# Optimization experiments

Hardware: AMD Instinct MI355X
Metric: run time of the kernel (lower is better)

The kernel has to match this reference:

```python
import math
import numpy as np
import jax, jax.numpy as jnp

L_MAX = 3
N_NODES = 16384
C_IN = 128
C_OUT = 128
IRREPS_DIM = (L_MAX + 1) ** 2  # 16 (dims 1+3+5+7, offset of l is l*l)


def _su2_cg(j1, j2, j3):
    """Complex-basis SU(2) Clebsch-Gordan <j1 m1 j2 m2 | j3 m3> (Racah formula)."""
    f = math.factorial
    C = np.zeros((2 * j1 + 1, 2 * j2 + 1, 2 * j3 + 1))
    for m1 in range(-j1, j1 + 1):
        for m2 in range(-j2, j2 + 1):
            m3 = m1 + m2
            if abs(m3) > j3:
                continue
            pref = math.sqrt((2 * j3 + 1) * f(j3 + j1 - j2) * f(j3 - j1 + j2) * f(j1 + j2 - j3) / f(j1 + j2 + j3 + 1))
            pref *= math.sqrt(f(j3 + m3) * f(j3 - m3) * f(j1 - m1) * f(j1 + m1) * f(j2 - m2) * f(j2 + m2))
            s = 0.0
            for k in range(0, j1 + j2 + 1):
                d = [k, j1 + j2 - j3 - k, j1 - m1 - k, j2 + m2 - k, j3 - j2 + m1 + k, j3 - j1 - m2 + k]
                if any(x < 0 for x in d):
                    continue
                s += (-1.0) ** k / (f(d[0]) * f(d[1]) * f(d[2]) * f(d[3]) * f(d[4]) * f(d[5]))
            C[m1 + j1, m2 + j2, m3 + j3] = pref * s
    return C


def _q(l):
    """Real->complex spherical-harmonic change of basis (e3nn convention, incl. (-i)^l)."""
    q = np.zeros((2 * l + 1, 2 * l + 1), dtype=complex)
    r2 = 1.0 / math.sqrt(2.0)
    for m in range(-l, 0):
        q[l + m, l + abs(m)] = r2
        q[l + m, l - abs(m)] = -1j * r2
    q[l, l] = 1.0
    for m in range(1, l + 1):
        q[l + m, l + abs(m)] = (-1) ** m * r2
        q[l + m, l - abs(m)] = 1j * (-1) ** m * r2
    return (-1j) ** l * q


def _real_cg(l1, l2, l3):
    """Real-basis Clebsch-Gordan tensor, shape (2l1+1, 2l2+1, 2l3+1). Real-valued."""
    C = _su2_cg(l1, l2, l3).astype(complex)
    W = np.einsum('ai,bj,ck,abc->ijk', _q(l1), _q(l2), _q(l3), C)
    return np.real(W).astype(np.float32)


# All triangle-allowed coupling paths (l1, l2, l_out); 34 paths for L_MAX=3.
PATHS = [(l1, l2, lo)
         for lo in range(L_MAX + 1)
         for l1 in range(L_MAX + 1)
         for l2 in range(L_MAX + 1)
         if abs(l1 - l2) <= lo <= l1 + l2]
NUM_PATHS = len(PATHS)
_counts = {}
for (_l1, _l2, _lo) in PATHS:
    _counts[_lo] = _counts.get(_lo, 0) + 1
# path_norm: divide each path by sqrt(#paths feeding its output irrep)
PATH_SCALE = [1.0 / math.sqrt(_counts[lo]) for (_, _, lo) in PATHS]
CG = {(l1, l2, lo): _real_cg(l1, l2, lo) for (l1, l2, lo) in PATHS}


def setup_inputs() -> dict:
    key = jax.random.key(0)
    k1, k2, k3 = jax.random.split(key, 3)
    input1 = jax.random.normal(k1, (N_NODES, IRREPS_DIM, C_IN), dtype=jnp.float32)
    input2 = jax.random.normal(k2, (N_NODES, IRREPS_DIM), dtype=jnp.float32)
    # uv-mode weight: (num_paths, channels_in, channels_out); fan-in init std=1/sqrt(C_IN)
    weight = jax.random.normal(k3, (NUM_PATHS, C_IN, C_OUT), dtype=jnp.float32) * (C_IN ** -0.5)
    return {"input1": input1, "input2": input2, "weight": weight}


def _forward(x1, x2, w):
    N = x1.shape[0]
    out = jnp.zeros((N, IRREPS_DIM, w.shape[-1]), dtype=x1.dtype)
    for p, (l1, l2, lo) in enumerate(PATHS):
        Cp = jnp.asarray(CG[(l1, l2, lo)], dtype=x1.dtype)      # (2l1+1, 2l2+1, 2lo+1)
        a = x1[:, l1 * l1:(l1 + 1) ** 2, :]                      # (N, 2l1+1, U)
        b = x2[:, l2 * l2:(l2 + 1) ** 2]                         # (N, 2l2+1)
        t = jnp.einsum('nau,nb,abc->ncu', a, b, Cp)              # (N, 2lo+1, U)
        o = jnp.einsum('ncu,uv->ncv', t, w[p]) * PATH_SCALE[p]   # (N, 2lo+1, V)
        out = out.at[:, lo * lo:(lo + 1) ** 2, :].add(o)
    return out


def reference(input1, input2, weight):
    return _forward(input1, input2, weight)
```

## Files before the change

kernel.cpp:

```cpp
#include <hip/hip_runtime.h>
#include <cstddef>

namespace so3 {

constexpr int IRR  = 16;
constexpr int CIN  = 128;
constexpr int COUT = 128;
constexpr int NP   = 34;
constexpr int NNODES = 16384;
constexpr int MT   = 16;

constexpr int H_L1[NP] = {0,1,2,3, 0,1,1,1,2,2,2,3,3, 0,1,1,1,2,2,2,2,3,3,3, 0,1,1,2,2,2,3,3,3,3};
constexpr int H_L2[NP] = {0,1,2,3, 1,0,1,2,1,2,3,2,3, 2,1,2,3,0,1,2,3,1,2,3, 3,2,3,1,2,3,0,1,2,3};
constexpr int H_START[4] = {0,4,13,24};
constexpr int H_CNT[4]   = {4,9,11,10};

constexpr double cfac(int n){ double r=1.0; for(int i=2;i<=n;++i) r *= (double)i; return r; }
constexpr double csqrt_(double x){
  if(x <= 0.0) return 0.0;
  double r = x < 1.0 ? 1.0 : x;
  for(int i=0;i<60;++i) r = 0.5*(r + x/r);
  return r;
}
constexpr double m1pow(int k){ return (k & 1) ? -1.0 : 1.0; }

struct CD { double re, im; };
constexpr CD cmul(CD a, CD b){ return CD{a.re*b.re - a.im*b.im, a.re*b.im + a.im*b.re}; }

struct CGDense { double v[7][7][7]; };
constexpr CGDense su2_cg(int j1,int j2,int j3){
  CGDense C{};
  for(int m1=-j1;m1<=j1;++m1){
    for(int m2=-j2;m2<=j2;++m2){
      int m3 = m1+m2;
      if(m3 < -j3 || m3 > j3) continue;
      double pref = csqrt_((2*j3+1) * cfac(j3+j1-j2)*cfac(j3-j1+j2)*cfac(j1+j2-j3)/cfac(j1+j2+j3+1));
      pref *= csqrt_(cfac(j3+m3)*cfac(j3-m3)*cfac(j1-m1)*cfac(j1+m1)*cfac(j2-m2)*cfac(j2+m2));
      double s = 0.0;
      for(int k=0;k<=j1+j2;++k){
        int d0=k, d1=j1+j2-j3-k, d2=j1-m1-k, d3=j2+m2-k, d4=j3-j2+m1+k, d5=j3-j1-m2+k;
        if(d0<0||d1<0||d2<0||d3<0||d4<0||d5<0) continue;
        s += m1pow(k)/(cfac(d0)*cfac(d1)*cfac(d2)*cfac(d3)*cfac(d4)*cfac(d5));
      }
      C.v[m1+j1][m2+j2][m3+j3] = pref*s;
    }
  }
  return C;
}

struct QMat { CD v[7][7]; };
constexpr QMat qmat(int l){
  QMat q{};
  const double r2 = 1.0/csqrt_(2.0);
  for(int m=-l;m<0;++m){
    q.v[l+m][l-m] = CD{r2, 0.0};
    q.v[l+m][l+m] = CD{0.0, -r2};
  }
  q.v[l][l] = CD{1.0, 0.0};
  for(int m=1;m<=l;++m){
    double sgn = m1pow(m);
    q.v[l+m][l+m] = CD{sgn*r2, 0.0};
    q.v[l+m][l-m] = CD{0.0, sgn*r2};
  }
  CD ph = CD{1.0, 0.0};
  int lm = l & 3;
  if(lm==1) ph = CD{0.0,-1.0};
  else if(lm==2) ph = CD{-1.0,0.0};
  else if(lm==3) ph = CD{0.0, 1.0};
  for(int i=0;i<2*l+1;++i)
    for(int j=0;j<2*l+1;++j)
      q.v[i][j] = cmul(q.v[i][j], ph);
  return q;
}

struct RealCG { double v[7][7][7]; };
constexpr RealCG real_cg(int l1,int l2,int l3){
  RealCG W{};
  const CGDense C = su2_cg(l1,l2,l3);
  const QMat q1 = qmat(l1), q2 = qmat(l2), q3 = qmat(l3);
  for(int i=0;i<2*l1+1;++i){
    int alist[2] = {i, 2*l1-i};
    int na = (alist[1]==alist[0]) ? 1 : 2;
    for(int j=0;j<2*l2+1;++j){
      int blist[2] = {j, 2*l2-j};
      int nb = (blist[1]==blist[0]) ? 1 : 2;
      for(int k=0;k<2*l3+1;++k){
        int clist[2] = {k, 2*l3-k};
        int nc = (clist[1]==clist[0]) ? 1 : 2;
        double re = 0.0;
        for(int ai=0;ai<na;++ai) for(int bi=0;bi<nb;++bi) for(int ci=0;ci<nc;++ci){
          int a=alist[ai], b=blist[bi], c=clist[ci];
          double cc = C.v[a][b][c];
          if(cc == 0.0) continue;
          CD t = cmul(cmul(q1.v[a][i], q2.v[b][j]), q3.v[c][k]);
          re += t.re * cc;
        }
        W.v[i][j][k] = re;
      }
    }
  }
  return W;
}

#define DECL_CG(n,a,b,c) constexpr RealCG CGP##n = real_cg(a,b,c);
DECL_CG(0,0,0,0)  DECL_CG(1,1,1,0)  DECL_CG(2,2,2,0)  DECL_CG(3,3,3,0)
DECL_CG(4,0,1,1)  DECL_CG(5,1,0,1)  DECL_CG(6,1,1,1)  DECL_CG(7,1,2,1)
DECL_CG(8,2,1,1)  DECL_CG(9,2,2,1)  DECL_CG(10,2,3,1) DECL_CG(11,3,2,1)
DECL_CG(12,3,3,1) DECL_CG(13,0,2,2) DECL_CG(14,1,1,2) DECL_CG(15,1,2,2)
DECL_CG(16,1,3,2) DECL_CG(17,2,0,2) DECL_CG(18,2,1,2) DECL_CG(19,2,2,2)
DECL_CG(20,2,3,2) DECL_CG(21,3,1,2) DECL_CG(22,3,2,2) DECL_CG(23,3,3,2)
DECL_CG(24,0,3,3) DECL_CG(25,1,2,3) DECL_CG(26,1,3,3) DECL_CG(27,2,1,3)
DECL_CG(28,2,2,3) DECL_CG(29,2,3,3) DECL_CG(30,3,0,3) DECL_CG(31,3,1,3)
DECL_CG(32,3,2,3) DECL_CG(33,3,3,3)
#undef DECL_CG

struct CGTable { float v[NP][7][7][7]; };
constexpr CGTable pack_cg(){
  const RealCG arr[NP] = {CGP0,CGP1,CGP2,CGP3,CGP4,CGP5,CGP6,CGP7,CGP8,CGP9,
                          CGP10,CGP11,CGP12,CGP13,CGP14,CGP15,CGP16,CGP17,CGP18,CGP19,
                          CGP20,CGP21,CGP22,CGP23,CGP24,CGP25,CGP26,CGP27,CGP28,CGP29,
                          CGP30,CGP31,CGP32,CGP33};
  CGTable t{};
  for(int p=0;p<NP;++p)
    for(int i=0;i<7;++i) for(int j=0;j<7;++j) for(int k=0;k<7;++k)
      t.v[p][i][j][k] = (float)arr[p].v[i][j][k];
  return t;
}

constexpr float PATH_SC[4] = {
  (float)(1.0/csqrt_((double)H_CNT[0])), (float)(1.0/csqrt_((double)H_CNT[1])),
  (float)(1.0/csqrt_((double)H_CNT[2])), (float)(1.0/csqrt_((double)H_CNT[3]))
};

}

__constant__ so3::CGTable c_cg = so3::pack_cg();

typedef __attribute__((ext_vector_type(8))) short bhalf8;
typedef __attribute__((ext_vector_type(4))) float floatx4;

__device__ __forceinline__ unsigned f2bf(float f){
  unsigned u = __builtin_bit_cast(unsigned, f);
  return (u + 0x7fffu + ((u>>16)&1u)) >> 16;
}

template<int LO, int PP>
__device__ __forceinline__ void path_iter(const int tid, const long n0,
    const float* __restrict__ x1, unsigned short* __restrict__ Tsh,
    float* __restrict__ gsh, const float* __restrict__ x2s,
    const unsigned short* __restrict__ wT,
    floatx4 (&acc)[16], bhalf8 (&bfrag)[4])
{
  using namespace so3;
  constexpr int NR  = 2*LO + 1;
  constexpr int CNT = H_CNT[LO];
  if constexpr (PP > CNT) { return; }
  else {
    const int lane = tid & 63;
    const int wv   = tid >> 6;
    const int lr   = lane & 15;
    const int lg   = lane >> 4;

    if constexpr (PP > 0) {
      constexpr int p = H_START[LO] + PP - 1;
      const unsigned short* wp = wT + p*16384 + (wv*16 + lr)*128 + lg*8;
      #pragma unroll
      for (int ks = 0; ks < 4; ++ks)
        bfrag[ks] = *(const bhalf8*)(wp + ks*32);
    }

    constexpr int n1_cur = (PP < CNT) ? (2*H_L1[H_START[LO] + (PP<CNT?PP:0)] + 1) : 1;
    float4 xf[n1_cur];
    const int bn = tid >> 5, u4 = tid & 31;
    if constexpr (PP < CNT) {
      constexpr int p  = H_START[LO] + PP;
      constexpr int l1 = H_L1[p];
      const float* x1p = x1 + ((size_t)(n0 + bn)*IRR + l1*l1)*CIN + u4*4;
      #pragma unroll
      for (int a = 0; a < n1_cur; ++a)
        xf[a] = *(const float4*)(x1p + a*CIN);
    }

    if constexpr (PP + 1 < CNT) {
      constexpr int p  = H_START[LO] + PP + 1;
      constexpr int l2 = H_L2[p];
      constexpr int n2 = 2*l2 + 1;
      constexpr int GT = NR*16*8;
      float* gout = gsh + ((PP+1)&1)*(7*16*8);
      #pragma unroll
      for (int e0 = 0; e0 < GT; e0 += 512) {
        const int e = e0 + tid;
        if (e < GT) {
          const int a = e & 7, n = (e >> 3) & 15, c = e >> 7;
          if (a < 2*H_L1[p] + 1) {
            float s = 0.f;
            #pragma unroll
            for (int b = 0; b < n2; ++b)
              s += c_cg.v[p][a][b][c] * x2s[n*16 + l2*l2 + b];
            gout[e] = s * PATH_SC[LO];
          }
        }
      }
    }

    if constexpr (PP < CNT) {
      const float* gin = gsh + (PP&1)*(7*16*8);
      char* Tbase = (char*)Tsh + (PP&1)*(7*16*128*2);
      #pragma unroll
      for (int c = 0; c < NR; ++c) {
        const float* g8 = gin + (c*16 + bn)*8;
        float garr[8];
        const float4 ga = *(const float4*)(g8);
        garr[0]=ga.x; garr[1]=ga.y; garr[2]=ga.z; garr[3]=ga.w;
        if constexpr (n1_cur > 4) {
          const float4 gb = *(const float4*)(g8 + 4);
          garr[4]=gb.x; garr[5]=gb.y; garr[6]=gb.z; garr[7]=gb.w;
        }
        float t0=0.f, t1=0.f, t2=0.f, t3=0.f;
        #pragma unroll
        for (int a = 0; a < n1_cur; ++a) {
          t0 += garr[a]*xf[a].x; t1 += garr[a]*xf[a].y;
          t2 += garr[a]*xf[a].z; t3 += garr[a]*xf[a].w;
        }
        uint2 o;
        o.x = f2bf(t0) | (f2bf(t1) << 16);
        o.y = f2bf(t2) | (f2bf(t3) << 16);
        const unsigned byte = ((unsigned)(((c*16 + bn)*128 + u4*4)*2)) ^ ((unsigned)((bn & 7) << 4));
        *(uint2*)(Tbase + byte) = o;
      }
    }

    if constexpr (PP > 0) {
      const char* Tbase = (const char*)Tsh + ((PP-1)&1)*(7*16*128*2);
      const unsigned xr = (unsigned)((lr & 7) << 4);
      #pragma unroll
      for (int c = 0; c < NR; ++c) {
        #pragma unroll
        for (int ks = 0; ks < 4; ++ks) {
          const unsigned byte = ((unsigned)((c*16 + lr)*256) + (unsigned)(ks*64 + lg*16)) ^ xr;
          bhalf8 av = *(const bhalf8*)(Tbase + byte);
          acc[LO*LO + c] = __builtin_amdgcn_mfma_f32_16x16x32_bf16(
              av, bfrag[ks], acc[LO*LO + c], 0, 0, 0);
        }
      }
    }
    __syncthreads();

    path_iter<LO, PP+1>(tid, n0, x1, Tsh, gsh, x2s, wT, acc, bfrag);
  }
}

template<int LO>
__device__ __forceinline__ void stage_a0(const int tid, float* __restrict__ gsh,
                                         const float* __restrict__ x2s)
{
  using namespace so3;
  constexpr int NR = 2*LO + 1;
  constexpr int p  = H_START[LO];
  constexpr int l1 = H_L1[p], l2 = H_L2[p];
  constexpr int n2 = 2*l2 + 1;
  constexpr int GT = NR*16*8;
  #pragma unroll
  for (int e0 = 0; e0 < GT; e0 += 512) {
    const int e = e0 + tid;
    if (e < GT) {
      const int a = e & 7, n = (e >> 3) & 15, c = e >> 7;
      if (a < 2*l1 + 1) {
        float s = 0.f;
        #pragma unroll
        for (int b = 0; b < n2; ++b)
          s += c_cg.v[p][a][b][c] * x2s[n*16 + l2*l2 + b];
        gsh[e] = s * PATH_SC[LO];
      }
    }
  }
}

__global__ __launch_bounds__(512, 4)
void so3_main(const float* __restrict__ x1, const float* __restrict__ x2,
              const unsigned short* __restrict__ wT, float* __restrict__ out)
{
  using namespace so3;
  __shared__ unsigned short Tsh[2*7*16*128];
  __shared__ float          gsh[2*7*16*8];
  __shared__ float          x2s[256];

  const int tid = threadIdx.x;
  const long n0 = (long)blockIdx.x * MT;

  if (tid < 256) x2s[tid] = x2[n0*16 + tid];
  __syncthreads();

  floatx4 acc[16];
  #pragma unroll
  for (int i = 0; i < 16; ++i) acc[i] = (floatx4){0.f,0.f,0.f,0.f};

  bhalf8 bfrag[4];

  stage_a0<0>(tid, gsh, x2s); __syncthreads();
  path_iter<0,0>(tid, n0, x1, Tsh, gsh, x2s, wT, acc, bfrag);
  stage_a0<1>(tid, gsh, x2s); __syncthreads();
  path_iter<1,0>(tid, n0, x1, Tsh, gsh, x2s, wT, acc, bfrag);
  stage_a0<2>(tid, gsh, x2s); __syncthreads();
  path_iter<2,0>(tid, n0, x1, Tsh, gsh, x2s, wT, acc, bfrag);
  stage_a0<3>(tid, gsh, x2s); __syncthreads();
  path_iter<3,0>(tid, n0, x1, Tsh, gsh, x2s, wT, acc, bfrag);

  const int lane = tid & 63, wv = tid >> 6, lr = lane & 15, lg = lane >> 4;
  const int v = wv*16 + lr;
  #pragma unroll
  for (int i = 0; i < 16; ++i) {
    #pragma unroll
    for (int r = 0; r < 4; ++r) {
      const long n = n0 + lg*4 + r;
      out[(n*16 + i)*128 + v] = acc[i][r];
    }
  }
}

__global__ void prep_wT(const float* __restrict__ w, unsigned short* __restrict__ wT)
{
  const int idx = blockIdx.x*256 + threadIdx.x;
  if (idx >= 34*128*128) return;
  const int p = idx >> 14, rem = idx & 16383, u = rem >> 7, v = rem & 127;
  wT[(p << 14) + (v << 7) + u] = (unsigned short)f2bf(w[idx]);
}

extern "C" void kernel_launch(void* const* d_in, const int* in_sizes, int n_in,
                              void* d_out, int out_size, void* d_ws, size_t ws_size,
                              hipStream_t stream)
{
  (void)in_sizes; (void)n_in; (void)out_size; (void)ws_size;
  const float* x1 = (const float*)d_in[0];
  const float* x2 = (const float*)d_in[1];
  const float* w  = (const float*)d_in[2];
  float* out = (float*)d_out;

  unsigned short* wT = (unsigned short*)d_ws;
  prep_wT<<<dim3(2176), dim3(256), 0, stream>>>(w, wT);
  so3_main<<<dim3(so3::NNODES / so3::MT), dim3(512), 0, stream>>>(x1, x2, wT, out);
}
```

Baseline: 317.4 us.

## Split kernel into two output-irrep pair launches with prefetched x1 and staged stores

The single fused kernel is split into two launches, one handling output irreps l=0 and l=3 and one handling l=1 and l=2, so each needs only 8 accumulator tiles instead of 16. This cuts register pressure and balances work between the two launches. x1 loads for the next path are now double-buffered in registers and issued ahead of the current path's compute. Output is staged through shared memory and written with coalesced float4 stores, and the block barrier is a custom waitcnt plus s_barrier. The cost is an extra launch, re-reading x2 and the weights in both launches, and a 64KB shared-memory footprint that may limit occupancy.

```diff
diff --git a/kernel.cpp b/kernel.cpp
--- a/kernel.cpp
+++ b/kernel.cpp
@@ -144,22 +144,60 @@
   return (u + 0x7fffu + ((u>>16)&1u)) >> 16;
 }
 
-template<int LO, int PP>
+#define SO3_BAR() do{ __builtin_amdgcn_sched_barrier(0); \
+  asm volatile("s_waitcnt lgkmcnt(0)" ::: "memory"); \
+  __builtin_amdgcn_s_barrier(); \
+  asm volatile("" ::: "memory"); \
+  __builtin_amdgcn_sched_barrier(0); }while(0)
+
+template<int LO>
+__device__ __forceinline__ void stage_a0(const int tid, const long n0,
+    const float* __restrict__ x1, float* __restrict__ gsh,
+    const float* __restrict__ x2s, float4 (&xf)[2][7])
+{
+  using namespace so3;
+  constexpr int NR = 2*LO + 1;
+  constexpr int p  = H_START[LO];
+  constexpr int l1 = H_L1[p], l2 = H_L2[p];
+  constexpr int n1 = 2*l1 + 1, n2 = 2*l2 + 1;
+  const int bn = tid >> 5, u4 = tid & 31;
+  const float* x1p = x1 + ((size_t)(n0 + bn)*IRR + l1*l1)*CIN + u4*4;
+  #pragma unroll
+  for (int a = 0; a < n1; ++a) xf[0][a] = *(const float4*)(x1p + a*CIN);
+
+  constexpr int GT = NR*16*8;
+  #pragma unroll
+  for (int e0 = 0; e0 < GT; e0 += 512) {
+    const int e = e0 + tid;
+    if (e < GT) {
+      const int a = e & 7, n = (e >> 3) & 15, c = e >> 7;
+      if (a < n1) {
+        float s = 0.f;
+        #pragma unroll
+        for (int b = 0; b < n2; ++b)
+          s += c_cg.v[p][a][b][c] * x2s[n*16 + l2*l2 + b];
+        gsh[e] = s * PATH_SC[LO];
+      }
+    }
+  }
+}
+
+template<int LO, int PP, int AOFF, int NIRR>
 __device__ __forceinline__ void path_iter(const int tid, const long n0,
     const float* __restrict__ x1, unsigned short* __restrict__ Tsh,
     float* __restrict__ gsh, const float* __restrict__ x2s,
     const unsigned short* __restrict__ wT,
-    floatx4 (&acc)[16], bhalf8 (&bfrag)[4])
+    floatx4 (&acc)[NIRR], bhalf8 (&bfrag)[4], float4 (&xf)[2][7])
 {
   using namespace so3;
   constexpr int NR  = 2*LO + 1;
   constexpr int CNT = H_CNT[LO];
+  constexpr int TS  = 7*16*128;
+  constexpr int GS  = 7*16*8;
   if constexpr (PP > CNT) { return; }
   else {
-    const int lane = tid & 63;
-    const int wv   = tid >> 6;
-    const int lr   = lane & 15;
-    const int lg   = lane >> 4;
+    const int lane = tid & 63, wv = tid >> 6, lr = lane & 15, lg = lane >> 4;
+    const int bn = tid >> 5, u4 = tid & 31;
 
     if constexpr (PP > 0) {
       constexpr int p = H_START[LO] + PP - 1;
@@ -169,30 +207,27 @@
         bfrag[ks] = *(const bhalf8*)(wp + ks*32);
     }
 
-    constexpr int n1_cur = (PP < CNT) ? (2*H_L1[H_START[LO] + (PP<CNT?PP:0)] + 1) : 1;
-    float4 xf[n1_cur];
-    const int bn = tid >> 5, u4 = tid & 31;
-    if constexpr (PP < CNT) {
-      constexpr int p  = H_START[LO] + PP;
-      constexpr int l1 = H_L1[p];
-      const float* x1p = x1 + ((size_t)(n0 + bn)*IRR + l1*l1)*CIN + u4*4;
-      #pragma unroll
-      for (int a = 0; a < n1_cur; ++a)
-        xf[a] = *(const float4*)(x1p + a*CIN);
+    if constexpr (PP + 1 < CNT) {
+      constexpr int p = H_START[LO] + PP + 1;
+      constexpr int l1n = H_L1[p]; constexpr int n1n = 2*l1n + 1;
+      const float* x1p = x1 + ((size_t)(n0 + bn)*IRR + l1n*l1n)*CIN + u4*4;
+      #pragma unroll
+      for (int a = 0; a < n1n; ++a)
+        xf[(PP+1)&1][a] = *(const float4*)(x1p + a*CIN);
     }
 
     if constexpr (PP + 1 < CNT) {
       constexpr int p  = H_START[LO] + PP + 1;
-      constexpr int l2 = H_L2[p];
+      constexpr int l1 = H_L1[p], l2 = H_L2[p];
       constexpr int n2 = 2*l2 + 1;
       constexpr int GT = NR*16*8;
-      float* gout = gsh + ((PP+1)&1)*(7*16*8);
+      float* gout = gsh + ((PP+1)&1)*GS;
       #pragma unroll
       for (int e0 = 0; e0 < GT; e0 += 512) {
         const int e = e0 + tid;
         if (e < GT) {
           const int a = e & 7, n = (e >> 3) & 15, c = e >> 7;
-          if (a < 2*H_L1[p] + 1) {
+          if (a < 2*l1 + 1) {
             float s = 0.f;
             #pragma unroll
             for (int b = 0; b < n2; ++b)
@@ -204,23 +239,26 @@
     }
 
     if constexpr (PP < CNT) {
-      const float* gin = gsh + (PP&1)*(7*16*8);
-      char* Tbase = (char*)Tsh + (PP&1)*(7*16*128*2);
+      constexpr int p  = H_START[LO] + PP;
+      constexpr int l1 = H_L1[p]; constexpr int n1 = 2*l1 + 1;
+      const float* gin = gsh + (PP&1)*GS;
+      char* Tbase = (char*)Tsh + (PP&1)*(TS*2);
       #pragma unroll
       for (int c = 0; c < NR; ++c) {
         const float* g8 = gin + (c*16 + bn)*8;
         float garr[8];
         const float4 ga = *(const float4*)(g8);
         garr[0]=ga.x; garr[1]=ga.y; garr[2]=ga.z; garr[3]=ga.w;
-        if constexpr (n1_cur > 4) {
+        if constexpr (n1 > 4) {
           const float4 gb = *(const float4*)(g8 + 4);
           garr[4]=gb.x; garr[5]=gb.y; garr[6]=gb.z; garr[7]=gb.w;
         }
         float t0=0.f, t1=0.f, t2=0.f, t3=0.f;
         #pragma unroll
-        for (int a = 0; a < n1_cur; ++a) {
-          t0 += garr[a]*xf[a].x; t1 += garr[a]*xf[a].y;
-          t2 += garr[a]*xf[a].z; t3 += garr[a]*xf[a].w;
+        for (int a = 0; a < n1; ++a) {
+          const float4 xa = xf[PP&1][a];
+          t0 += garr[a]*xa.x; t1 += garr[a]*xa.y;
+          t2 += garr[a]*xa.z; t3 += garr[a]*xa.w;
         }
         uint2 o;
         o.x = f2bf(t0) | (f2bf(t1) << 16);
@@ -231,7 +269,7 @@
     }
 
     if constexpr (PP > 0) {
-      const char* Tbase = (const char*)Tsh + ((PP-1)&1)*(7*16*128*2);
+      const char* Tbase = (const char*)Tsh + ((PP-1)&1)*(TS*2);
       const unsigned xr = (unsigned)((lr & 7) << 4);
       #pragma unroll
       for (int c = 0; c < NR; ++c) {
@@ -239,51 +277,28 @@
         for (int ks = 0; ks < 4; ++ks) {
           const unsigned byte = ((unsigned)((c*16 + lr)*256) + (unsigned)(ks*64 + lg*16)) ^ xr;
           bhalf8 av = *(const bhalf8*)(Tbase + byte);
-          acc[LO*LO + c] = __builtin_amdgcn_mfma_f32_16x16x32_bf16(
-              av, bfrag[ks], acc[LO*LO + c], 0, 0, 0);
-        }
-      }
-    }
-    __syncthreads();
-
-    path_iter<LO, PP+1>(tid, n0, x1, Tsh, gsh, x2s, wT, acc, bfrag);
-  }
-}
-
-template<int LO>
-__device__ __forceinline__ void stage_a0(const int tid, float* __restrict__ gsh,
-                                         const float* __restrict__ x2s)
+          acc[AOFF + c] = __builtin_amdgcn_mfma_f32_16x16x32_bf16(
+              av, bfrag[ks], acc[AOFF + c], 0, 0, 0);
+        }
+      }
+    }
+
+    SO3_BAR();
+    path_iter<LO, PP+1, AOFF, NIRR>(tid, n0, x1, Tsh, gsh, x2s, wT, acc, bfrag, xf);
+  }
+}
+
+template<int LOA, int LOB>
+__global__ __launch_bounds__(512, 4)
+void so3_pair(const float* __restrict__ x1, const float* __restrict__ x2,
+              const unsigned short* __restrict__ wT, float* __restrict__ out)
 {
   using namespace so3;
-  constexpr int NR = 2*LO + 1;
-  constexpr int p  = H_START[LO];
-  constexpr int l1 = H_L1[p], l2 = H_L2[p];
-  constexpr int n2 = 2*l2 + 1;
-  constexpr int GT = NR*16*8;
-  #pragma unroll
-  for (int e0 = 0; e0 < GT; e0 += 512) {
-    const int e = e0 + tid;
-    if (e < GT) {
-      const int a = e & 7, n = (e >> 3) & 15, c = e >> 7;
-      if (a < 2*l1 + 1) {
-        float s = 0.f;
-        #pragma unroll
-        for (int b = 0; b < n2; ++b)
-          s += c_cg.v[p][a][b][c] * x2s[n*16 + l2*l2 + b];
-        gsh[e] = s * PATH_SC[LO];
-      }
-    }
-  }
-}
-
-__global__ __launch_bounds__(512, 4)
-void so3_main(const float* __restrict__ x1, const float* __restrict__ x2,
-              const unsigned short* __restrict__ wT, float* __restrict__ out)
-{
-  using namespace so3;
-  __shared__ unsigned short Tsh[2*7*16*128];
-  __shared__ float          gsh[2*7*16*8];
-  __shared__ float          x2s[256];
+  constexpr int NRA = 2*LOA + 1, NRB = 2*LOB + 1, NIRR = NRA + NRB;
+  __shared__ __align__(16) char smem[65536];
+  unsigned short* Tsh = (unsigned short*)smem;
+  float* gsh = (float*)(smem + 57344);
+  float* x2s = (float*)(smem + 57344 + 7168);
 
   const int tid = threadIdx.x;
   const long n0 = (long)blockIdx.x * MT;
@@ -291,29 +306,43 @@
   if (tid < 256) x2s[tid] = x2[n0*16 + tid];
   __syncthreads();
 
-  floatx4 acc[16];
+  floatx4 acc[NIRR];
   #pragma unroll
-  for (int i = 0; i < 16; ++i) acc[i] = (floatx4){0.f,0.f,0.f,0.f};
-
+  for (int i = 0; i < NIRR; ++i) acc[i] = (floatx4){0.f,0.f,0.f,0.f};
   bhalf8 bfrag[4];
-
-  stage_a0<0>(tid, gsh, x2s); __syncthreads();
-  path_iter<0,0>(tid, n0, x1, Tsh, gsh, x2s, wT, acc, bfrag);
-  stage_a0<1>(tid, gsh, x2s); __syncthreads();
-  path_iter<1,0>(tid, n0, x1, Tsh, gsh, x2s, wT, acc, bfrag);
-  stage_a0<2>(tid, gsh, x2s); __syncthreads();
-  path_iter<2,0>(tid, n0, x1, Tsh, gsh, x2s, wT, acc, bfrag);
-  stage_a0<3>(tid, gsh, x2s); __syncthreads();
-  path_iter<3,0>(tid, n0, x1, Tsh, gsh, x2s, wT, acc, bfrag);
-
+  float4 xf[2][7];
+
+  stage_a0<LOA>(tid, n0, x1, gsh, x2s, xf);
+  __syncthreads();
+  path_iter<LOA, 0, 0, NIRR>(tid, n0, x1, Tsh, gsh, x2s, wT, acc, bfrag, xf);
+  __syncthreads();
+  stage_a0<LOB>(tid, n0, x1, gsh, x2s, xf);
+  __syncthreads();
+  path_iter<LOB, 0, NRA, NIRR>(tid, n0, x1, Tsh, gsh, x2s, wT, acc, bfrag, xf);
+  __syncthreads();
+
+  float* epi = (float*)smem;
   const int lane = tid & 63, wv = tid >> 6, lr = lane & 15, lg = lane >> 4;
   const int v = wv*16 + lr;
   #pragma unroll
-  for (int i = 0; i < 16; ++i) {
+  for (int ch = 0; ch < 2; ++ch) {
+    if (ch) __syncthreads();
     #pragma unroll
-    for (int r = 0; r < 4; ++r) {
-      const long n = n0 + lg*4 + r;
-      out[(n*16 + i)*128 + v] = acc[i][r];
+    for (int ii = 0; ii < 4; ++ii) {
+      #pragma unroll
+      for (int r = 0; r < 4; ++r)
+        epi[(ii*16 + lg*4 + r)*132 + v] = acc[ch*4 + ii][r];
+    }
+    __syncthreads();
+    #pragma unroll
+    for (int j = 0; j < 4; ++j) {
+      const int k   = tid + j*512;
+      const int row = k >> 5, c4 = k & 31;
+      const int n   = row >> 2, ii = row & 3;
+      const int idx = ch*4 + ii;
+      const int gi  = (idx < NRA) ? (LOA*LOA + idx) : (LOB*LOB + idx - NRA);
+      const float4 val = *(const float4*)(epi + (ii*16 + n)*132 + c4*4);
+      *(float4*)(out + ((n0 + n)*16 + gi)*128 + c4*4) = val;
     }
   }
 }
@@ -338,5 +367,6 @@
 
   unsigned short* wT = (unsigned short*)d_ws;
   prep_wT<<<dim3(2176), dim3(256), 0, stream>>>(w, wT);
-  so3_main<<<dim3(so3::NNODES / so3::MT), dim3(512), 0, stream>>>(x1, x2, wT, out);
-}
+  so3_pair<0,3><<<dim3(so3::NNODES / so3::MT), dim3(512), 0, stream>>>(x1, x2, wT, out);
+  so3_pair<1,2><<<dim3(so3::NNODES / so3::MT), dim3(512), 0, stream>>>(x1, x2, wT, out);
+}
```

New measurement: 487.4 us. 53.6% more time.
